# Performance work log

Hardware: AMD Instinct MI355X
Metric: run time of the kernel (lower is better)

## Reference

```python
import jax, jax.numpy as jnp
import numpy as np

B = 262144
D = 16          # input_dim
D2 = D // 2     # 8, == hidden_dim
H = 8           # hidden_dim
L = 15          # num_layers (couplings)
NH = 3          # hidden_block_layers
EPS = 1e-6
SLOPE = 0.01    # LeakyReLU default


def setup_inputs() -> dict:
    key = jax.random.key(0)
    ks = jax.random.split(key, 8)
    z = jax.random.normal(ks[0], (B, D), dtype=jnp.float32)
    s = 0.2  # keep log_s away from the +/-5 clamp saturation
    W_in = jax.random.normal(ks[1], (L, 2, D2, H), dtype=jnp.float32) * s
    b_in = jax.random.normal(ks[2], (L, 2, H), dtype=jnp.float32) * s
    W_hid = jax.random.normal(ks[3], (L, 2, NH, H, H), dtype=jnp.float32) * s
    b_hid = jax.random.normal(ks[4], (L, 2, NH, H), dtype=jnp.float32) * s
    W_out = jax.random.normal(ks[5], (L, 2, H, D2), dtype=jnp.float32) * s
    b_out = jax.random.normal(ks[6], (L, 2, D2), dtype=jnp.float32) * s
    # 14 random permutations between couplings + identity after the last coupling
    rng = np.random.default_rng(0)
    perms = np.stack([rng.permutation(D) for _ in range(L - 1)] + [np.arange(D)])
    perms = jnp.asarray(perms, dtype=jnp.int32)  # [L, D]
    return {"z": z, "W_in": W_in, "b_in": b_in, "W_hid": W_hid,
            "b_hid": b_hid, "W_out": W_out, "b_out": b_out, "perms": perms}


def _mlp(x, Wi, bi, Wh, bh, Wo, bo):
    # LinearBlock: (Linear+LeakyReLU) + NH x (Linear+LeakyReLU) + Linear
    h = jax.nn.leaky_relu(x @ Wi + bi, SLOPE)
    for j in range(NH):  # NH is a small static constant
        h = jax.nn.leaky_relu(h @ Wh[j] + bh[j], SLOPE)
    return h @ Wo + bo


def _flow(z, W_in, b_in, W_hid, b_hid, W_out, b_out, perms):
    def step(carry, params):
        z, ld = carry
        Wi, bi, Wh, bh, Wo, bo, perm = params
        z_l, z_r = z[:, :D2], z[:, D2:]
        log_s = jnp.clip(_mlp(z_l, Wi[0], bi[0], Wh[0], bh[0], Wo[0], bo[0]), -5.0, 5.0)
        b = _mlp(z_l, Wi[1], bi[1], Wh[1], bh[1], Wo[1], bo[1])
        y_r = (jnp.exp(log_s) + EPS) * z_r + b
        y = jnp.concatenate([z_l, y_r], axis=1)
        ld = ld + jnp.sum(log_s, axis=1)
        y = y[:, perm]  # Permutation layer (identity for the last step)
        return (y, ld), None

    ld0 = jnp.zeros(z.shape[0], dtype=z.dtype)
    (y, ld), _ = jax.lax.scan(step, (z, ld0), (W_in, b_in, W_hid, b_hid, W_out, b_out, perms))
    return y, ld


def reference(z, W_in, b_in, W_hid, b_hid, W_out, b_out, perms):
    return _flow(z, W_in, b_in, W_hid, b_hid, W_out, b_out, perms)
```

## Files before the change

### kernel.cpp

```cpp
#include <hip/hip_runtime.h>

#define BN 262144
#define HALF (BN / 2)
#define LNUM 15
#define NSTG 151
#define NF4 (NSTG * 18)
#define LOG2E 1.4426950408889634f
#define LN2 0.6931471805599453f
#define L2CLIP 7.2134752044448170f

extern "C" __global__ void build_slab(
    const float* __restrict__ Wi, const float* __restrict__ bi,
    const float* __restrict__ Wh, const float* __restrict__ bh,
    const float* __restrict__ Wo, const float* __restrict__ bo,
    float* __restrict__ slab) {
    int idx = blockIdx.x * 256 + threadIdx.x;
    if (idx >= NSTG * 72) return;
    int sl = idx / 72, k = idx % 72;
    if (sl == NSTG - 1) sl = 0;
    const int l = sl / 10, r = sl % 10, net = r / 5, st = r % 5;
    const int nb = l * 2 + net;
    const float sc = (net == 0 && st == 4) ? LOG2E : 1.0f;
    float v;
    if (k < 8) {
        if (st == 0)      v = bi[nb * 8 + k];
        else if (st < 4)  v = bh[(nb * 3 + (st - 1)) * 8 + k];
        else              v = bo[nb * 8 + k] * sc;
    } else {
        const int kk = k - 8;
        if (st == 0)      v = Wi[nb * 64 + kk];
        else if (st < 4)  v = Wh[(nb * 3 + (st - 1)) * 64 + kk];
        else              v = Wo[nb * 64 + kk] * sc;
    }
    slab[idx] = v;
}

extern "C" __global__ void compose_perms(const int* __restrict__ perms, int* __restrict__ c) {
    if (threadIdx.x != 0 || blockIdx.x != 0) return;
    int cur[16];
    for (int j = 0; j < 16; ++j) { cur[j] = j; c[j] = j; }
    for (int l = 0; l < LNUM; ++l) {
        int nx[16];
        for (int j = 0; j < 16; ++j) nx[j] = cur[perms[l * 16 + j]];
        for (int j = 0; j < 16; ++j) { c[(l + 1) * 16 + j] = nx[j]; cur[j] = nx[j]; }
    }
}

#define GB(gb, k) ((k) % 4 == 0 ? gb[(k) / 4].x : (k) % 4 == 1 ? gb[(k) / 4].y \
                 : (k) % 4 == 2 ? gb[(k) / 4].z : gb[(k) / 4].w)

#define CHA(IN, OUT, BUF)                                                     \
    {                                                                         \
        _Pragma("unroll") for (int o = 0; o < 8; ++o) {                       \
            const float bb = GB(BUF, o);                                      \
            const float w0 = GB(BUF, 8 + o), w1 = GB(BUF, 16 + o);            \
            _Pragma("unroll") for (int s = 0; s < 2; ++s)                     \
                OUT[s][o] = fmaf(IN[s][1], w1, fmaf(IN[s][0], w0, bb));       \
        }                                                                     \
        _Pragma("unroll") for (int j = 0; j < 6; ++j) BUF[j] = gptr[j];       \
        gptr += 6;                                                            \
        __builtin_amdgcn_sched_barrier(0);                                    \
    }
#define CHB(IN, OUT, BUF)                                                     \
    {                                                                         \
        _Pragma("unroll") for (int o = 0; o < 8; ++o) {                       \
            const float w2 = GB(BUF, o), w3 = GB(BUF, 8 + o), w4 = GB(BUF, 16 + o); \
            _Pragma("unroll") for (int s = 0; s < 2; ++s)                     \
                OUT[s][o] = fmaf(IN[s][4], w4,                                 \
                             fmaf(IN[s][3], w3, fmaf(IN[s][2], w2, OUT[s][o]))); \
        }                                                                     \
        _Pragma("unroll") for (int j = 0; j < 6; ++j) BUF[j] = gptr[j];       \
        gptr += 6;                                                            \
        __builtin_amdgcn_sched_barrier(0);                                    \
    }
#define CHC(IN, OUT, BUF, DOLR)                                               \
    {                                                                         \
        _Pragma("unroll") for (int o = 0; o < 8; ++o) {                       \
            const float w5 = GB(BUF, o), w6 = GB(BUF, 8 + o), w7 = GB(BUF, 16 + o); \
            _Pragma("unroll") for (int s = 0; s < 2; ++s) {                   \
                float a = fmaf(IN[s][7], w7,                                   \
                            fmaf(IN[s][6], w6, fmaf(IN[s][5], w5, OUT[s][o]))); \
                OUT[s][o] = (DOLR) ? fmaxf(a, 0.01f * a) : a;                 \
            }                                                                 \
        }                                                                     \
        _Pragma("unroll") for (int j = 0; j < 6; ++j) BUF[j] = gptr[j];       \
        gptr += 6;                                                            \
        __builtin_amdgcn_sched_barrier(0);                                    \
    }
#define STG(IN, OUT, DOLR) CHA(IN, OUT, B0) CHB(IN, OUT, B1) CHC(IN, OUT, B2, DOLR)

extern "C" __global__ void __launch_bounds__(512) flow_fwd(
    const float* __restrict__ z, const float* __restrict__ slab,
    const int* __restrict__ cperm,
    float* __restrict__ outy, float* __restrict__ outld) {
    __shared__ float4 wls[NF4];
    __shared__ float xs[512 * 33];
    const int t = threadIdx.x;
    const long i = (long)blockIdx.x * 512 + t;
    float* __restrict__ myx = &xs[t * 33];

    {
        const float4* gs = reinterpret_cast<const float4*>(slab);
        for (int k = t; k < NF4; k += 512) wls[k] = gs[k];
    }
    {
        const float4* zp = reinterpret_cast<const float4*>(z + i * 16);
        const float4* zq = reinterpret_cast<const float4*>(z + (i + HALF) * 16);
#pragma unroll
        for (int q = 0; q < 4; ++q) {
            float4 a = zp[q], b = zq[q];
            myx[4 * q] = a.x; myx[4 * q + 1] = a.y; myx[4 * q + 2] = a.z; myx[4 * q + 3] = a.w;
            myx[16 + 4 * q] = b.x; myx[17 + 4 * q] = b.y; myx[18 + 4 * q] = b.z; myx[19 + 4 * q] = b.w;
        }
    }
    float ld2A = 0.f, ld2B = 0.f;
    __syncthreads();

    float4 B0[6], B1[6], B2[6];
#pragma unroll
    for (int j = 0; j < 6; ++j) { B0[j] = wls[j]; B1[j] = wls[6 + j]; B2[j] = wls[12 + j]; }
    const float4* gptr = wls + 18;
    __builtin_amdgcn_sched_barrier(0);

#pragma unroll 1
    for (int l = 0; l < LNUM; ++l) {
        const int* __restrict__ cl = cperm + l * 16;
        float in2[2][8];
#pragma unroll
        for (int j = 0; j < 8; ++j) {
            const int off = cl[j];
            in2[0][j] = myx[off];
            in2[1][j] = myx[16 + off];
        }
        float h[2][8], g[2][8], sf[2][8], bf[2][8];
        STG(in2, h, 1) STG(h, g, 1) STG(g, h, 1) STG(h, g, 1) STG(g, sf, 0)
        STG(in2, h, 1) STG(h, g, 1) STG(g, h, 1) STG(h, g, 1) STG(g, bf, 0)

#pragma unroll
        for (int k = 0; k < 8; ++k) {
            const int off = cl[8 + k];
            const float cA = fminf(fmaxf(sf[0][k], -L2CLIP), L2CLIP);
            const float cB = fminf(fmaxf(sf[1][k], -L2CLIP), L2CLIP);
            ld2A += cA; ld2B += cB;
            myx[off]      = fmaf(__builtin_amdgcn_exp2f(cA) + 1e-6f, myx[off],      bf[0][k]);
            myx[16 + off] = fmaf(__builtin_amdgcn_exp2f(cB) + 1e-6f, myx[16 + off], bf[1][k]);
        }
    }

    {
        const int* __restrict__ cf = cperm + LNUM * 16;
        float4 oa[4], ob[4];
#pragma unroll
        for (int q = 0; q < 4; ++q) {
            const int c0 = cf[4 * q], c1 = cf[4 * q + 1], c2 = cf[4 * q + 2], c3 = cf[4 * q + 3];
            oa[q].x = myx[c0]; oa[q].y = myx[c1]; oa[q].z = myx[c2]; oa[q].w = myx[c3];
            ob[q].x = myx[16 + c0]; ob[q].y = myx[16 + c1];
            ob[q].z = myx[16 + c2]; ob[q].w = myx[16 + c3];
        }
        float4* ya = reinterpret_cast<float4*>(outy + i * 16);
        float4* yb = reinterpret_cast<float4*>(outy + (i + HALF) * 16);
#pragma unroll
        for (int q = 0; q < 4; ++q) { ya[q] = oa[q]; yb[q] = ob[q]; }
        outld[i] = ld2A * LN2;
        outld[i + HALF] = ld2B * LN2;
    }
}

extern "C" void kernel_launch(void* const* d_in, const int* in_sizes, int n_in,
                              void* d_out, int out_size, void* d_ws, size_t ws_size,
                              hipStream_t stream) {
    const float* z = (const float*)d_in[0];
    const float* Wi = (const float*)d_in[1];
    const float* bi = (const float*)d_in[2];
    const float* Wh = (const float*)d_in[3];
    const float* bh = (const float*)d_in[4];
    const float* Wo = (const float*)d_in[5];
    const float* bo = (const float*)d_in[6];
    const int* perms = (const int*)d_in[7];
    float* out = (float*)d_out;
    float* slab = (float*)d_ws;
    int* cperm = (int*)(slab + NSTG * 72);

    hipLaunchKernelGGL(build_slab, dim3((NSTG * 72 + 255) / 256), dim3(256), 0, stream,
                       Wi, bi, Wh, bh, Wo, bo, slab);
    hipLaunchKernelGGL(compose_perms, dim3(1), dim3(64), 0, stream, perms, cperm);
    hipLaunchKernelGGL(flow_fwd, dim3(HALF / 512), dim3(512), 0, stream,
                       z, slab, cperm, out, out + (size_t)BN * 16);
}
```

Before: 95.93 us.

## Broadcast MLP weights via readlane from per-lane registers instead of LDS reads

Each lane now loads one weight element of the current stage into a VGPR, double-buffered across stages. The weights are broadcast to the wave with v_readlane instead of every thread reading float4 weight chunks from LDS. This is meant to reduce LDS bandwidth and the VGPRs held for weight buffers. The trade-off is an extra readlane instruction per weight, which adds issue pressure next to the FMAs.

Measured after the change: 155.8 us. +62.4%, slower.

```diff
diff --git a/kernel.cpp b/kernel.cpp
--- a/kernel.cpp
+++ b/kernel.cpp
@@ -46,62 +46,46 @@
     }
 }
 
-#define GB(gb, k) ((k) % 4 == 0 ? gb[(k) / 4].x : (k) % 4 == 1 ? gb[(k) / 4].y \
-                 : (k) % 4 == 2 ? gb[(k) / 4].z : gb[(k) / 4].w)
+#define RL(v, j) __uint_as_float(__builtin_amdgcn_readlane(__float_as_uint(v), (j)))
 
-#define CHA(IN, OUT, BUF)                                                     \
-    {                                                                         \
-        _Pragma("unroll") for (int o = 0; o < 8; ++o) {                       \
-            const float bb = GB(BUF, o);                                      \
-            const float w0 = GB(BUF, 8 + o), w1 = GB(BUF, 16 + o);            \
-            _Pragma("unroll") for (int s = 0; s < 2; ++s)                     \
-                OUT[s][o] = fmaf(IN[s][1], w1, fmaf(IN[s][0], w0, bb));       \
-        }                                                                     \
-        _Pragma("unroll") for (int j = 0; j < 6; ++j) BUF[j] = gptr[j];       \
-        gptr += 6;                                                            \
-        __builtin_amdgcn_sched_barrier(0);                                    \
+#define STG(IN, OUT, DOLR, VC0, VC1, VN0, VN1, NXTOFF)                         \
+    {                                                                          \
+        VN0 = w0p[NXTOFF];                                                     \
+        VN1 = w1p[NXTOFF];                                                     \
+        _Pragma("unroll") for (int o = 0; o < 8; ++o) {                        \
+            const float bb = RL(VC0, o);                                       \
+            OUT[0][o] = bb; OUT[1][o] = bb;                                    \
+        }                                                                      \
+        _Pragma("unroll") for (int ii = 0; ii < 7; ++ii)                       \
+            _Pragma("unroll") for (int o = 0; o < 8; ++o) {                    \
+                const float w = RL(VC0, 8 + ii * 8 + o);                       \
+                OUT[0][o] = fmaf(IN[0][ii], w, OUT[0][o]);                     \
+                OUT[1][o] = fmaf(IN[1][ii], w, OUT[1][o]);                     \
+            }                                                                  \
+        _Pragma("unroll") for (int o = 0; o < 8; ++o) {                        \
+            const float w = RL(VC1, o);                                        \
+            const float a0 = fmaf(IN[0][7], w, OUT[0][o]);                     \
+            const float a1 = fmaf(IN[1][7], w, OUT[1][o]);                     \
+            OUT[0][o] = (DOLR) ? fmaxf(a0, 0.01f * a0) : a0;                   \
+            OUT[1][o] = (DOLR) ? fmaxf(a1, 0.01f * a1) : a1;                   \
+        }                                                                      \
     }
-#define CHB(IN, OUT, BUF)                                                     \
-    {                                                                         \
-        _Pragma("unroll") for (int o = 0; o < 8; ++o) {                       \
-            const float w2 = GB(BUF, o), w3 = GB(BUF, 8 + o), w4 = GB(BUF, 16 + o); \
-            _Pragma("unroll") for (int s = 0; s < 2; ++s)                     \
-                OUT[s][o] = fmaf(IN[s][4], w4,                                 \
-                             fmaf(IN[s][3], w3, fmaf(IN[s][2], w2, OUT[s][o]))); \
-        }                                                                     \
-        _Pragma("unroll") for (int j = 0; j < 6; ++j) BUF[j] = gptr[j];       \
-        gptr += 6;                                                            \
-        __builtin_amdgcn_sched_barrier(0);                                    \
-    }
-#define CHC(IN, OUT, BUF, DOLR)                                               \
-    {                                                                         \
-        _Pragma("unroll") for (int o = 0; o < 8; ++o) {                       \
-            const float w5 = GB(BUF, o), w6 = GB(BUF, 8 + o), w7 = GB(BUF, 16 + o); \
-            _Pragma("unroll") for (int s = 0; s < 2; ++s) {                   \
-                float a = fmaf(IN[s][7], w7,                                   \
-                            fmaf(IN[s][6], w6, fmaf(IN[s][5], w5, OUT[s][o]))); \
-                OUT[s][o] = (DOLR) ? fmaxf(a, 0.01f * a) : a;                 \
-            }                                                                 \
-        }                                                                     \
-        _Pragma("unroll") for (int j = 0; j < 6; ++j) BUF[j] = gptr[j];       \
-        gptr += 6;                                                            \
-        __builtin_amdgcn_sched_barrier(0);                                    \
-    }
-#define STG(IN, OUT, DOLR) CHA(IN, OUT, B0) CHB(IN, OUT, B1) CHC(IN, OUT, B2, DOLR)
 
 extern "C" __global__ void __launch_bounds__(512) flow_fwd(
     const float* __restrict__ z, const float* __restrict__ slab,
     const int* __restrict__ cperm,
     float* __restrict__ outy, float* __restrict__ outld) {
-    __shared__ float4 wls[NF4];
+    __shared__ float wls[NSTG * 72];
     __shared__ float xs[512 * 33];
     const int t = threadIdx.x;
+    const int lane = t & 63;
     const long i = (long)blockIdx.x * 512 + t;
     float* __restrict__ myx = &xs[t * 33];
 
     {
+        float4* wd = reinterpret_cast<float4*>(wls);
         const float4* gs = reinterpret_cast<const float4*>(slab);
-        for (int k = t; k < NF4; k += 512) wls[k] = gs[k];
+        for (int k = t; k < NF4; k += 512) wd[k] = gs[k];
     }
     {
         const float4* zp = reinterpret_cast<const float4*>(z + i * 16);
@@ -116,15 +100,14 @@
     float ld2A = 0.f, ld2B = 0.f;
     __syncthreads();
 
-    float4 B0[6], B1[6], B2[6];
-#pragma unroll
-    for (int j = 0; j < 6; ++j) { B0[j] = wls[j]; B1[j] = wls[6 + j]; B2[j] = wls[12 + j]; }
-    const float4* gptr = wls + 18;
-    __builtin_amdgcn_sched_barrier(0);
+    float vA0 = wls[lane], vA1 = wls[64 + (lane & 7)];
+    float vB0, vB1;
 
 #pragma unroll 1
     for (int l = 0; l < LNUM; ++l) {
         const int* __restrict__ cl = cperm + l * 16;
+        const float* __restrict__ w0p = wls + l * 720 + lane;
+        const float* __restrict__ w1p = wls + l * 720 + 64 + (lane & 7);
         float in2[2][8];
 #pragma unroll
         for (int j = 0; j < 8; ++j) {
@@ -133,8 +116,16 @@
             in2[1][j] = myx[16 + off];
         }
         float h[2][8], g[2][8], sf[2][8], bf[2][8];
-        STG(in2, h, 1) STG(h, g, 1) STG(g, h, 1) STG(h, g, 1) STG(g, sf, 0)
-        STG(in2, h, 1) STG(h, g, 1) STG(g, h, 1) STG(h, g, 1) STG(g, bf, 0)
+        STG(in2, h, 1, vA0, vA1, vB0, vB1, 1 * 72)
+        STG(h, g, 1,   vB0, vB1, vA0, vA1, 2 * 72)
+        STG(g, h, 1,   vA0, vA1, vB0, vB1, 3 * 72)
+        STG(h, g, 1,   vB0, vB1, vA0, vA1, 4 * 72)
+        STG(g, sf, 0,  vA0, vA1, vB0, vB1, 5 * 72)
+        STG(in2, h, 1, vB0, vB1, vA0, vA1, 6 * 72)
+        STG(h, g, 1,   vA0, vA1, vB0, vB1, 7 * 72)
+        STG(g, h, 1,   vB0, vB1, vA0, vA1, 8 * 72)
+        STG(h, g, 1,   vA0, vA1, vB0, vB1, 9 * 72)
+        STG(g, bf, 0,  vB0, vB1, vA0, vA1, 10 * 72)
 
 #pragma unroll
         for (int k = 0; k < 8; ++k) {
```

## Process four samples per thread with full-stage weight double-buffering in registers

Applied to the files above, without the earlier changes.

Each thread now handles four batch rows instead of two, so every weight value loaded from LDS is reused across four samples. Whole-stage weights (18 float4) are double-buffered in registers and pinned with inline asm, replacing the three-chunk rotation. Blocks shrink to 256 threads with launch bounds of one block per CU, and the per-thread shared scratch stride grows to 65. The cost is much higher register pressure and lower occupancy, which risks spills and less latency hiding.

Result: slower. 138.4 us (+44.3%).

```diff
diff --git a/kernel.cpp b/kernel.cpp
--- a/kernel.cpp
+++ b/kernel.cpp
@@ -1,13 +1,16 @@
 #include <hip/hip_runtime.h>
 
 #define BN 262144
-#define HALF (BN / 2)
+#define S4 4
+#define QS (BN / S4)
 #define LNUM 15
 #define NSTG 151
 #define NF4 (NSTG * 18)
 #define LOG2E 1.4426950408889634f
 #define LN2 0.6931471805599453f
 #define L2CLIP 7.2134752044448170f
+
+typedef __attribute__((ext_vector_type(4))) float f4;
 
 extern "C" __global__ void build_slab(
     const float* __restrict__ Wi, const float* __restrict__ bi,
@@ -46,123 +49,124 @@
     }
 }
 
-#define GB(gb, k) ((k) % 4 == 0 ? gb[(k) / 4].x : (k) % 4 == 1 ? gb[(k) / 4].y \
-                 : (k) % 4 == 2 ? gb[(k) / 4].z : gb[(k) / 4].w)
+#define GBX(W, k) (W[(k) / 4][(k) % 4])
 
-#define CHA(IN, OUT, BUF)                                                     \
+#define PINW(W) asm volatile("" : "+v"(W[0]),"+v"(W[1]),"+v"(W[2]),"+v"(W[3]), \
+    "+v"(W[4]),"+v"(W[5]),"+v"(W[6]),"+v"(W[7]),"+v"(W[8]),"+v"(W[9]),        \
+    "+v"(W[10]),"+v"(W[11]),"+v"(W[12]),"+v"(W[13]),"+v"(W[14]),"+v"(W[15]),  \
+    "+v"(W[16]),"+v"(W[17]))
+
+#define PREF_PIN(W, SIDX)                                                     \
     {                                                                         \
-        _Pragma("unroll") for (int o = 0; o < 8; ++o) {                       \
-            const float bb = GB(BUF, o);                                      \
-            const float w0 = GB(BUF, 8 + o), w1 = GB(BUF, 16 + o);            \
-            _Pragma("unroll") for (int s = 0; s < 2; ++s)                     \
-                OUT[s][o] = fmaf(IN[s][1], w1, fmaf(IN[s][0], w0, bb));       \
-        }                                                                     \
-        _Pragma("unroll") for (int j = 0; j < 6; ++j) BUF[j] = gptr[j];       \
-        gptr += 6;                                                            \
+        const f4* sp = &wls[(SIDX) * 18];                                     \
+        _Pragma("unroll") for (int j = 0; j < 18; ++j) W[j] = sp[j];          \
+        PINW(W);                                                              \
         __builtin_amdgcn_sched_barrier(0);                                    \
     }
-#define CHB(IN, OUT, BUF)                                                     \
-    {                                                                         \
+
+#define MV(IN, OUT, W, LR)                                                    \
+    _Pragma("unroll") for (int o = 0; o < 8; ++o) {                           \
+        const float w0 = GBX(W, 8 + o), bb = GBX(W, o);                       \
+        _Pragma("unroll") for (int s = 0; s < 4; ++s)                         \
+            OUT[s][o] = fmaf(IN[s][0], w0, bb);                               \
+    }                                                                         \
+    _Pragma("unroll") for (int i2 = 1; i2 < 8; ++i2)                          \
         _Pragma("unroll") for (int o = 0; o < 8; ++o) {                       \
-            const float w2 = GB(BUF, o), w3 = GB(BUF, 8 + o), w4 = GB(BUF, 16 + o); \
-            _Pragma("unroll") for (int s = 0; s < 2; ++s)                     \
-                OUT[s][o] = fmaf(IN[s][4], w4,                                 \
-                             fmaf(IN[s][3], w3, fmaf(IN[s][2], w2, OUT[s][o]))); \
+            const float w = GBX(W, 8 + i2 * 8 + o);                           \
+            _Pragma("unroll") for (int s = 0; s < 4; ++s)                     \
+                OUT[s][o] = fmaf(IN[s][i2], w, OUT[s][o]);                    \
         }                                                                     \
-        _Pragma("unroll") for (int j = 0; j < 6; ++j) BUF[j] = gptr[j];       \
-        gptr += 6;                                                            \
-        __builtin_amdgcn_sched_barrier(0);                                    \
+    if (LR) {                                                                 \
+        _Pragma("unroll") for (int s = 0; s < 4; ++s)                         \
+            _Pragma("unroll") for (int o = 0; o < 8; ++o)                     \
+                OUT[s][o] = fmaxf(OUT[s][o], 0.01f * OUT[s][o]);              \
     }
-#define CHC(IN, OUT, BUF, DOLR)                                               \
-    {                                                                         \
-        _Pragma("unroll") for (int o = 0; o < 8; ++o) {                       \
-            const float w5 = GB(BUF, o), w6 = GB(BUF, 8 + o), w7 = GB(BUF, 16 + o); \
-            _Pragma("unroll") for (int s = 0; s < 2; ++s) {                   \
-                float a = fmaf(IN[s][7], w7,                                   \
-                            fmaf(IN[s][6], w6, fmaf(IN[s][5], w5, OUT[s][o]))); \
-                OUT[s][o] = (DOLR) ? fmaxf(a, 0.01f * a) : a;                 \
-            }                                                                 \
-        }                                                                     \
-        _Pragma("unroll") for (int j = 0; j < 6; ++j) BUF[j] = gptr[j];       \
-        gptr += 6;                                                            \
-        __builtin_amdgcn_sched_barrier(0);                                    \
-    }
-#define STG(IN, OUT, DOLR) CHA(IN, OUT, B0) CHB(IN, OUT, B1) CHC(IN, OUT, B2, DOLR)
 
-extern "C" __global__ void __launch_bounds__(512) flow_fwd(
+#define STGM(IN, OUT, LR, PB, PIDX, CB) PREF_PIN(PB, PIDX) MV(IN, OUT, CB, LR)
+
+extern "C" __global__ void __launch_bounds__(256, 1) flow_fwd(
     const float* __restrict__ z, const float* __restrict__ slab,
     const int* __restrict__ cperm,
     float* __restrict__ outy, float* __restrict__ outld) {
-    __shared__ float4 wls[NF4];
-    __shared__ float xs[512 * 33];
+    __shared__ f4 wls[NF4];
+    __shared__ float xs[256 * 65];
     const int t = threadIdx.x;
-    const long i = (long)blockIdx.x * 512 + t;
-    float* __restrict__ myx = &xs[t * 33];
+    const int i0 = blockIdx.x * 256 + t;
+    float* __restrict__ myx = &xs[t * 65];
 
     {
-        const float4* gs = reinterpret_cast<const float4*>(slab);
-        for (int k = t; k < NF4; k += 512) wls[k] = gs[k];
+        const f4* gs = reinterpret_cast<const f4*>(slab);
+        for (int k = t; k < NF4; k += 256) wls[k] = gs[k];
     }
-    {
-        const float4* zp = reinterpret_cast<const float4*>(z + i * 16);
-        const float4* zq = reinterpret_cast<const float4*>(z + (i + HALF) * 16);
+#pragma unroll
+    for (int s = 0; s < 4; ++s) {
+        const float4* zp = reinterpret_cast<const float4*>(z + (long)(i0 + s * QS) * 16);
 #pragma unroll
         for (int q = 0; q < 4; ++q) {
-            float4 a = zp[q], b = zq[q];
-            myx[4 * q] = a.x; myx[4 * q + 1] = a.y; myx[4 * q + 2] = a.z; myx[4 * q + 3] = a.w;
-            myx[16 + 4 * q] = b.x; myx[17 + 4 * q] = b.y; myx[18 + 4 * q] = b.z; myx[19 + 4 * q] = b.w;
+            float4 a = zp[q];
+            myx[s * 16 + 4 * q] = a.x; myx[s * 16 + 4 * q + 1] = a.y;
+            myx[s * 16 + 4 * q + 2] = a.z; myx[s * 16 + 4 * q + 3] = a.w;
         }
     }
-    float ld2A = 0.f, ld2B = 0.f;
+    float ld[4] = {0.f, 0.f, 0.f, 0.f};
     __syncthreads();
 
-    float4 B0[6], B1[6], B2[6];
-#pragma unroll
-    for (int j = 0; j < 6; ++j) { B0[j] = wls[j]; B1[j] = wls[6 + j]; B2[j] = wls[12 + j]; }
-    const float4* gptr = wls + 18;
-    __builtin_amdgcn_sched_barrier(0);
+    f4 WA[18], WB[18];
+    PREF_PIN(WA, 0)
 
 #pragma unroll 1
     for (int l = 0; l < LNUM; ++l) {
         const int* __restrict__ cl = cperm + l * 16;
-        float in2[2][8];
+        const int base = l * 10;
+        float in2[4][8];
 #pragma unroll
         for (int j = 0; j < 8; ++j) {
             const int off = cl[j];
-            in2[0][j] = myx[off];
-            in2[1][j] = myx[16 + off];
+#pragma unroll
+            for (int s = 0; s < 4; ++s) in2[s][j] = myx[s * 16 + off];
         }
-        float h[2][8], g[2][8], sf[2][8], bf[2][8];
-        STG(in2, h, 1) STG(h, g, 1) STG(g, h, 1) STG(h, g, 1) STG(g, sf, 0)
-        STG(in2, h, 1) STG(h, g, 1) STG(g, h, 1) STG(h, g, 1) STG(g, bf, 0)
+        float h[4][8], g[4][8], sf[4][8], bf[4][8];
+        STGM(in2, h, 1, WB, base + 1, WA)
+        STGM(h, g, 1,   WA, base + 2, WB)
+        STGM(g, h, 1,   WB, base + 3, WA)
+        STGM(h, g, 1,   WA, base + 4, WB)
+        STGM(g, sf, 0,  WB, base + 5, WA)
+        STGM(in2, h, 1, WA, base + 6, WB)
+        STGM(h, g, 1,   WB, base + 7, WA)
+        STGM(g, h, 1,   WA, base + 8, WB)
+        STGM(h, g, 1,   WB, base + 9, WA)
+        STGM(g, bf, 0,  WA, base + 10, WB)
 
 #pragma unroll
         for (int k = 0; k < 8; ++k) {
             const int off = cl[8 + k];
-            const float cA = fminf(fmaxf(sf[0][k], -L2CLIP), L2CLIP);
-            const float cB = fminf(fmaxf(sf[1][k], -L2CLIP), L2CLIP);
-            ld2A += cA; ld2B += cB;
-            myx[off]      = fmaf(__builtin_amdgcn_exp2f(cA) + 1e-6f, myx[off],      bf[0][k]);
-            myx[16 + off] = fmaf(__builtin_amdgcn_exp2f(cB) + 1e-6f, myx[16 + off], bf[1][k]);
+#pragma unroll
+            for (int s = 0; s < 4; ++s) {
+                const float cs = fminf(fmaxf(sf[s][k], -L2CLIP), L2CLIP);
+                ld[s] += cs;
+                myx[s * 16 + off] = fmaf(__builtin_amdgcn_exp2f(cs) + 1e-6f,
+                                         myx[s * 16 + off], bf[s][k]);
+            }
         }
     }
 
     {
         const int* __restrict__ cf = cperm + LNUM * 16;
-        float4 oa[4], ob[4];
 #pragma unroll
-        for (int q = 0; q < 4; ++q) {
-            const int c0 = cf[4 * q], c1 = cf[4 * q + 1], c2 = cf[4 * q + 2], c3 = cf[4 * q + 3];
-            oa[q].x = myx[c0]; oa[q].y = myx[c1]; oa[q].z = myx[c2]; oa[q].w = myx[c3];
-            ob[q].x = myx[16 + c0]; ob[q].y = myx[16 + c1];
-            ob[q].z = myx[16 + c2]; ob[q].w = myx[16 + c3];
+        for (int s = 0; s < 4; ++s) {
+            float4 o[4];
+#pragma unroll
+            for (int q = 0; q < 4; ++q) {
+                o[q].x = myx[s * 16 + cf[4 * q]];
+                o[q].y = myx[s * 16 + cf[4 * q + 1]];
+                o[q].z = myx[s * 16 + cf[4 * q + 2]];
+                o[q].w = myx[s * 16 + cf[4 * q + 3]];
+            }
+            float4* ya = reinterpret_cast<float4*>(outy + (long)(i0 + s * QS) * 16);
+#pragma unroll
+            for (int q = 0; q < 4; ++q) ya[q] = o[q];
+            outld[i0 + s * QS] = ld[s] * LN2;
         }
-        float4* ya = reinterpret_cast<float4*>(outy + i * 16);
-        float4* yb = reinterpret_cast<float4*>(outy + (i + HALF) * 16);
-#pragma unroll
-        for (int q = 0; q < 4; ++q) { ya[q] = oa[q]; yb[q] = ob[q]; }
-        outld[i] = ld2A * LN2;
-        outld[i + HALF] = ld2B * LN2;
     }
 }
 
@@ -184,6 +188,6 @@
     hipLaunchKernelGGL(build_slab, dim3((NSTG * 72 + 255) / 256), dim3(256), 0, stream,
                        Wi, bi, Wh, bh, Wo, bo, slab);
     hipLaunchKernelGGL(compose_perms, dim3(1), dim3(64), 0, stream, perms, cperm);
-    hipLaunchKernelGGL(flow_fwd, dim3(HALF / 512), dim3(512), 0, stream,
+    hipLaunchKernelGGL(flow_fwd, dim3(QS / 256), dim3(256), 0, stream,
                        z, slab, cperm, out, out + (size_t)BN * 16);
 }
```

## Read translation-net weights from global memory as uniform scalar loads instead of LDS

Applied to the files above, without the earlier changes.

The weight slab is split into two parts. Only the log-scale network's stages stay in LDS with the rotating float4 register buffers. The translation network's weights now sit in a separate global region and are read directly through uniform-address loads (MVS macro), which the compiler can turn into scalar SMEM loads. This roughly halves LDS footprint and LDS read traffic per layer, at the cost of relying on scalar cache hits and compiler scalarization; the vector-type change is cosmetic.

Measured after the change: 102.7 us. +7.0%, slower.

```diff
diff --git a/kernel.cpp b/kernel.cpp
--- a/kernel.cpp
+++ b/kernel.cpp
@@ -3,11 +3,14 @@
 #define BN 262144
 #define HALF (BN / 2)
 #define LNUM 15
-#define NSTG 151
-#define NF4 (NSTG * 18)
+#define NSTG0 76
+#define NF4 (NSTG0 * 18)
+#define NTOT ((NSTG0 + 75) * 72)
 #define LOG2E 1.4426950408889634f
 #define LN2 0.6931471805599453f
 #define L2CLIP 7.2134752044448170f
+
+typedef __attribute__((ext_vector_type(4))) float f4;
 
 extern "C" __global__ void build_slab(
     const float* __restrict__ Wi, const float* __restrict__ bi,
@@ -15,10 +18,16 @@
     const float* __restrict__ Wo, const float* __restrict__ bo,
     float* __restrict__ slab) {
     int idx = blockIdx.x * 256 + threadIdx.x;
-    if (idx >= NSTG * 72) return;
-    int sl = idx / 72, k = idx % 72;
-    if (sl == NSTG - 1) sl = 0;
-    const int l = sl / 10, r = sl % 10, net = r / 5, st = r % 5;
+    if (idx >= NTOT) return;
+    int sl, k, net;
+    if (idx < NSTG0 * 72) {
+        sl = idx / 72; k = idx % 72; net = 0;
+        if (sl == NSTG0 - 1) sl = 0;
+    } else {
+        const int j = idx - NSTG0 * 72;
+        sl = j / 72; k = j % 72; net = 1;
+    }
+    const int l = sl / 5, st = sl % 5;
     const int nb = l * 2 + net;
     const float sc = (net == 0 && st == 4) ? LOG2E : 1.0f;
     float v;
@@ -46,8 +55,7 @@
     }
 }
 
-#define GB(gb, k) ((k) % 4 == 0 ? gb[(k) / 4].x : (k) % 4 == 1 ? gb[(k) / 4].y \
-                 : (k) % 4 == 2 ? gb[(k) / 4].z : gb[(k) / 4].w)
+#define GB(gb, k) (gb[(k) / 4][(k) % 4])
 
 #define CHA(IN, OUT, BUF)                                                     \
     {                                                                         \
@@ -89,18 +97,38 @@
     }
 #define STG(IN, OUT, DOLR) CHA(IN, OUT, B0) CHB(IN, OUT, B1) CHC(IN, OUT, B2, DOLR)
 
+#define MVS(IN, OUT, W, DOLR)                                                 \
+    {                                                                         \
+        _Pragma("unroll") for (int o = 0; o < 8; ++o) {                       \
+            const float bb = (W)[o];                                          \
+            OUT[0][o] = bb; OUT[1][o] = bb;                                   \
+        }                                                                     \
+        _Pragma("unroll") for (int i2 = 0; i2 < 8; ++i2)                      \
+            _Pragma("unroll") for (int o = 0; o < 8; ++o) {                   \
+                const float w = (W)[8 + i2 * 8 + o];                          \
+                OUT[0][o] = fmaf(IN[0][i2], w, OUT[0][o]);                    \
+                OUT[1][o] = fmaf(IN[1][i2], w, OUT[1][o]);                    \
+            }                                                                 \
+        if (DOLR) {                                                           \
+            _Pragma("unroll") for (int s = 0; s < 2; ++s)                     \
+                _Pragma("unroll") for (int o = 0; o < 8; ++o)                 \
+                    OUT[s][o] = fmaxf(OUT[s][o], 0.01f * OUT[s][o]);          \
+        }                                                                     \
+    }
+
 extern "C" __global__ void __launch_bounds__(512) flow_fwd(
     const float* __restrict__ z, const float* __restrict__ slab,
     const int* __restrict__ cperm,
     float* __restrict__ outy, float* __restrict__ outld) {
-    __shared__ float4 wls[NF4];
+    __shared__ f4 wls[NF4];
     __shared__ float xs[512 * 33];
     const int t = threadIdx.x;
     const long i = (long)blockIdx.x * 512 + t;
     float* __restrict__ myx = &xs[t * 33];
+    const float* __restrict__ gw1 = slab + NSTG0 * 72;
 
     {
-        const float4* gs = reinterpret_cast<const float4*>(slab);
+        const f4* gs = reinterpret_cast<const f4*>(slab);
         for (int k = t; k < NF4; k += 512) wls[k] = gs[k];
     }
     {
@@ -116,15 +144,16 @@
     float ld2A = 0.f, ld2B = 0.f;
     __syncthreads();
 
-    float4 B0[6], B1[6], B2[6];
+    f4 B0[6], B1[6], B2[6];
 #pragma unroll
     for (int j = 0; j < 6; ++j) { B0[j] = wls[j]; B1[j] = wls[6 + j]; B2[j] = wls[12 + j]; }
-    const float4* gptr = wls + 18;
+    const f4* gptr = wls + 18;
     __builtin_amdgcn_sched_barrier(0);
 
 #pragma unroll 1
     for (int l = 0; l < LNUM; ++l) {
         const int* __restrict__ cl = cperm + l * 16;
+        const float* __restrict__ w1 = gw1 + l * 360;
         float in2[2][8];
 #pragma unroll
         for (int j = 0; j < 8; ++j) {
@@ -134,7 +163,11 @@
         }
         float h[2][8], g[2][8], sf[2][8], bf[2][8];
         STG(in2, h, 1) STG(h, g, 1) STG(g, h, 1) STG(h, g, 1) STG(g, sf, 0)
-        STG(in2, h, 1) STG(h, g, 1) STG(g, h, 1) STG(h, g, 1) STG(g, bf, 0)
+        MVS(in2, h, w1 + 0, 1)
+        MVS(h, g, w1 + 72, 1)
+        MVS(g, h, w1 + 144, 1)
+        MVS(h, g, w1 + 216, 1)
+        MVS(g, bf, w1 + 288, 0)
 
 #pragma unroll
         for (int k = 0; k < 8; ++k) {
@@ -179,9 +212,9 @@
     const int* perms = (const int*)d_in[7];
     float* out = (float*)d_out;
     float* slab = (float*)d_ws;
-    int* cperm = (int*)(slab + NSTG * 72);
-
-    hipLaunchKernelGGL(build_slab, dim3((NSTG * 72 + 255) / 256), dim3(256), 0, stream,
+    int* cperm = (int*)(slab + NTOT);
+
+    hipLaunchKernelGGL(build_slab, dim3((NTOT + 255) / 256), dim3(256), 0, stream,
                        Wi, bi, Wh, bh, Wo, bo, slab);
     hipLaunchKernelGGL(compose_perms, dim3(1), dim3(64), 0, stream, perms, cperm);
     hipLaunchKernelGGL(flow_fwd, dim3(HALF / 512), dim3(512), 0, stream,
```
